# Kernel optimization log

Measured on AMD Instinct MI355X. Metric: run time of the kernel, lower is better.

The kernel has to match this reference:

```python
import jax, jax.numpy as jnp
import numpy as np

BETA = 0.5
THRESHOLD = 1e-12
NORM_EPS = 1e-12
SQRT_EPS = 1e-12


def _l2_normalize(x):
    # matches torch F.normalize(p=2, dim=1, eps=1e-12): x / max(||x||, eps)
    n = jnp.sqrt(jnp.sum(x * x, axis=1, keepdims=True))
    return x / jnp.maximum(n, NORM_EPS)


def _focal(d):
    # reg_method='log': log(beta*d + 1) if d > threshold else 0
    d_safe = jnp.where(d > THRESHOLD, d, THRESHOLD)
    return jnp.where(d > THRESHOLD, jnp.log(BETA * d_safe + 1.0), 0.0)


def setup_inputs() -> dict:
    key = jax.random.key(0)
    ks = jax.random.split(key, 6)
    B, D = 128, 512
    return {
        "x_audio": jax.random.normal(ks[0], (B, D), dtype=jnp.float32),
        "x_video": jax.random.normal(ks[1], (B, D), dtype=jnp.float32),
        "x_text": jax.random.normal(ks[2], (B, D), dtype=jnp.float32),
        "loss_audio": jax.random.uniform(ks[3], (), dtype=jnp.float32),
        "loss_video": jax.random.uniform(ks[4], (), dtype=jnp.float32),
        "loss_text": jax.random.uniform(ks[5], (), dtype=jnp.float32),
    }


def reference(x_audio, x_video, x_text, loss_audio, loss_video, loss_text):
    xs = [x_audio, x_video, x_text]
    losses = [loss_audio, loss_video, loss_text]
    R = len(xs)
    # L2-normalize each modality, then per-sample outer-product correlations [B, D, D]
    corr = [jnp.einsum('bi,bj->bij', xn, xn)
            for xn in (_l2_normalize(x) for x in xs)]
    ssa = []
    for m in range(R):
        acc = jnp.float32(0.0)
        for n in range(R):
            focal = _focal(losses[m] - losses[n])
            diff = corr[m] - corr[n]
            corr_diff = jnp.sqrt(SQRT_EPS + jnp.sum(diff * diff))
            acc = acc + focal * corr_diff
        ssa.append(acc)
    return jnp.stack(ssa)  # [R] ssa loss per modality
```

## Files before the change

### kernel.cpp

```cpp
#include <hip/hip_runtime.h>
#include <math.h>


#define SSA_BETA      0.5f
#define SSA_THRESHOLD 1e-12f
#define SSA_NORM_EPS  1e-12f
#define SSA_SQRT_EPS  1e-12f

static constexpr int SSA_B = 128;
static constexpr int SSA_D = 512;
static constexpr int SSA_NBLK = 32;
static constexpr int SSA_CTR_OFS = 512;

__global__ __launch_bounds__(256) void ssa_fused_kernel(
    const float* __restrict__ xa, const float* __restrict__ xv,
    const float* __restrict__ xt, const float* __restrict__ la,
    const float* __restrict__ lv, const float* __restrict__ lt,
    float* __restrict__ out, float* __restrict__ ws) {
  const int tid = threadIdx.x;
  const int wave = tid >> 6;
  const int lane = tid & 63;
  const int b = blockIdx.x * 4 + wave;

  const float4* pa = reinterpret_cast<const float4*>(xa + b * SSA_D);
  const float4* pv = reinterpret_cast<const float4*>(xv + b * SSA_D);
  const float4* pt = reinterpret_cast<const float4*>(xt + b * SSA_D);

  float sa = 0.f, sv = 0.f, st = 0.f;
  float dav = 0.f, dat = 0.f, dvt = 0.f;

#pragma unroll
  for (int k = 0; k < 2; ++k) {
    const int idx = lane + 64 * k;
    const float4 a = pa[idx];
    const float4 v = pv[idx];
    const float4 t = pt[idx];
    sa  += a.x * a.x + a.y * a.y + a.z * a.z + a.w * a.w;
    sv  += v.x * v.x + v.y * v.y + v.z * v.z + v.w * v.w;
    st  += t.x * t.x + t.y * t.y + t.z * t.z + t.w * t.w;
    dav += a.x * v.x + a.y * v.y + a.z * v.z + a.w * v.w;
    dat += a.x * t.x + a.y * t.y + a.z * t.z + a.w * t.w;
    dvt += v.x * t.x + v.y * t.y + v.z * t.z + v.w * t.w;
  }

#pragma unroll
  for (int off = 32; off > 0; off >>= 1) {
    sa  += __shfl_xor(sa, off);
    sv  += __shfl_xor(sv, off);
    st  += __shfl_xor(st, off);
    dav += __shfl_xor(dav, off);
    dat += __shfl_xor(dat, off);
    dvt += __shfl_xor(dvt, off);
  }

  __shared__ float sm[3][4];
  if (lane == 0) {
    const float na = fmaxf(sqrtf(sa), SSA_NORM_EPS);
    const float nv = fmaxf(sqrtf(sv), SSA_NORM_EPS);
    const float nt = fmaxf(sqrtf(st), SSA_NORM_EPS);
    const float na2 = sa / (na * na);
    const float nv2 = sv / (nv * nv);
    const float nt2 = st / (nt * nt);
    const float cav  = dav / (na * nv);
    const float cat_ = dat / (na * nt);
    const float cvt_ = dvt / (nv * nt);
    sm[0][wave] = na2 * na2 + nv2 * nv2 - 2.f * cav  * cav;
    sm[1][wave] = na2 * na2 + nt2 * nt2 - 2.f * cat_ * cat_;
    sm[2][wave] = nv2 * nv2 + nt2 * nt2 - 2.f * cvt_ * cvt_;
  }
  __syncthreads();

  if (wave != 0) return;

  unsigned int old = 0;
  if (lane == 0) {
    ws[0 * SSA_NBLK + blockIdx.x] = sm[0][0] + sm[0][1] + sm[0][2] + sm[0][3];
    ws[1 * SSA_NBLK + blockIdx.x] = sm[1][0] + sm[1][1] + sm[1][2] + sm[1][3];
    ws[2 * SSA_NBLK + blockIdx.x] = sm[2][0] + sm[2][1] + sm[2][2] + sm[2][3];
    __threadfence();
    old = atomicAdd(reinterpret_cast<unsigned int*>(ws + SSA_CTR_OFS), 1u);
  }
  old = __shfl(old, 0);
  if ((old & 31u) != 31u) return;

  __threadfence();

  float s0 = 0.f, s1 = 0.f, s2 = 0.f;
  if (lane < SSA_NBLK) {
    s0 = ws[0 * SSA_NBLK + lane];
    s1 = ws[1 * SSA_NBLK + lane];
    s2 = ws[2 * SSA_NBLK + lane];
  }
#pragma unroll
  for (int off = 16; off > 0; off >>= 1) {
    s0 += __shfl_xor(s0, off);
    s1 += __shfl_xor(s1, off);
    s2 += __shfl_xor(s2, off);
  }

  if (lane == 0) {
    const float dist01 = sqrtf(SSA_SQRT_EPS + s0);
    const float dist02 = sqrtf(SSA_SQRT_EPS + s1);
    const float dist12 = sqrtf(SSA_SQRT_EPS + s2);

    const float loss[3] = {la[0], lv[0], lt[0]};
    const float dist[3][3] = {{0.f, dist01, dist02},
                              {dist01, 0.f, dist12},
                              {dist02, dist12, 0.f}};
#pragma unroll
    for (int m = 0; m < 3; ++m) {
      float acc = 0.f;
#pragma unroll
      for (int n = 0; n < 3; ++n) {
        if (n == m) continue;
        const float d = loss[m] - loss[n];
        const float focal = (d > SSA_THRESHOLD) ? logf(SSA_BETA * d + 1.0f) : 0.f;
        acc += focal * dist[m][n];
      }
      out[m] = acc;
    }
  }
}

extern "C" void kernel_launch(void* const* d_in, const int* in_sizes, int n_in,
                              void* d_out, int out_size, void* d_ws, size_t ws_size,
                              hipStream_t stream) {
  const float* xa = (const float*)d_in[0];
  const float* xv = (const float*)d_in[1];
  const float* xt = (const float*)d_in[2];
  const float* la = (const float*)d_in[3];
  const float* lv = (const float*)d_in[4];
  const float* lt = (const float*)d_in[5];
  float* out = (float*)d_out;
  float* ws = (float*)d_ws;

  ssa_fused_kernel<<<SSA_NBLK, 256, 0, stream>>>(xa, xv, xt, la, lv, lt, out, ws);
}
```

Baseline: 9.753 us.

## Halve block count, hoist focal computation, and reset counter via memset

Launches 16 blocks of 512 threads (8 samples per block) instead of 32 blocks of 256, so fewer blocks take part in the last-block atomic reduction. The loss scalars and focal logs are computed early by every thread, overlapping with the vector loads instead of sitting on the serial tail of the last block. The per-block partial sums are reduced by shuffles, and the counter is now reset with a hipMemsetAsync before each launch. The exact-equality check on the counter replaces the modulo test. The extra memset node may add launch overhead that offsets the smaller tail work.

```diff
diff --git a/kernel.cpp b/kernel.cpp
--- a/kernel.cpp
+++ b/kernel.cpp
@@ -9,10 +9,10 @@
 
 static constexpr int SSA_B = 128;
 static constexpr int SSA_D = 512;
-static constexpr int SSA_NBLK = 32;
+static constexpr int SSA_NBLK = 16;
 static constexpr int SSA_CTR_OFS = 512;
 
-__global__ __launch_bounds__(256) void ssa_fused_kernel(
+__global__ __launch_bounds__(512) void ssa_fused_kernel(
     const float* __restrict__ xa, const float* __restrict__ xv,
     const float* __restrict__ xt, const float* __restrict__ la,
     const float* __restrict__ lv, const float* __restrict__ lt,
@@ -20,7 +20,9 @@
   const int tid = threadIdx.x;
   const int wave = tid >> 6;
   const int lane = tid & 63;
-  const int b = blockIdx.x * 4 + wave;
+  const int b = blockIdx.x * 8 + wave;
+
+  const float l0 = la[0], l1 = lv[0], l2 = lt[0];
 
   const float4* pa = reinterpret_cast<const float4*>(xa + b * SSA_D);
   const float4* pv = reinterpret_cast<const float4*>(xv + b * SSA_D);
@@ -43,6 +45,13 @@
     dvt += v.x * t.x + v.y * t.y + v.z * t.z + v.w * t.w;
   }
 
+  auto focal = [](float d) {
+    return (d > SSA_THRESHOLD) ? logf(SSA_BETA * d + 1.0f) : 0.f;
+  };
+  const float f01 = focal(l0 - l1), f10 = focal(l1 - l0);
+  const float f02 = focal(l0 - l2), f20 = focal(l2 - l0);
+  const float f12 = focal(l1 - l2), f21 = focal(l2 - l1);
+
 #pragma unroll
   for (int off = 32; off > 0; off >>= 1) {
     sa  += __shfl_xor(sa, off);
@@ -53,7 +62,7 @@
     dvt += __shfl_xor(dvt, off);
   }
 
-  __shared__ float sm[3][4];
+  __shared__ float sm[3][8];
   if (lane == 0) {
     const float na = fmaxf(sqrtf(sa), SSA_NORM_EPS);
     const float nv = fmaxf(sqrtf(sv), SSA_NORM_EPS);
@@ -72,16 +81,22 @@
 
   if (wave != 0) return;
 
+  const int pair = lane >> 3;
+  float pv_ = (pair < 3) ? sm[pair][lane & 7] : 0.f;
+#pragma unroll
+  for (int off = 4; off > 0; off >>= 1) pv_ += __shfl_xor(pv_, off);
+  if (pair < 3 && (lane & 7) == 0) {
+    ws[pair * SSA_NBLK + blockIdx.x] = pv_;
+  }
+
+  __threadfence();
+
   unsigned int old = 0;
   if (lane == 0) {
-    ws[0 * SSA_NBLK + blockIdx.x] = sm[0][0] + sm[0][1] + sm[0][2] + sm[0][3];
-    ws[1 * SSA_NBLK + blockIdx.x] = sm[1][0] + sm[1][1] + sm[1][2] + sm[1][3];
-    ws[2 * SSA_NBLK + blockIdx.x] = sm[2][0] + sm[2][1] + sm[2][2] + sm[2][3];
-    __threadfence();
     old = atomicAdd(reinterpret_cast<unsigned int*>(ws + SSA_CTR_OFS), 1u);
   }
   old = __shfl(old, 0);
-  if ((old & 31u) != 31u) return;
+  if (old != (unsigned int)(SSA_NBLK - 1)) return;
 
   __threadfence();
 
@@ -92,7 +107,7 @@
     s2 = ws[2 * SSA_NBLK + lane];
   }
 #pragma unroll
-  for (int off = 16; off > 0; off >>= 1) {
+  for (int off = 8; off > 0; off >>= 1) {
     s0 += __shfl_xor(s0, off);
     s1 += __shfl_xor(s1, off);
     s2 += __shfl_xor(s2, off);
@@ -102,23 +117,9 @@
     const float dist01 = sqrtf(SSA_SQRT_EPS + s0);
     const float dist02 = sqrtf(SSA_SQRT_EPS + s1);
     const float dist12 = sqrtf(SSA_SQRT_EPS + s2);
-
-    const float loss[3] = {la[0], lv[0], lt[0]};
-    const float dist[3][3] = {{0.f, dist01, dist02},
-                              {dist01, 0.f, dist12},
-                              {dist02, dist12, 0.f}};
-#pragma unroll
-    for (int m = 0; m < 3; ++m) {
-      float acc = 0.f;
-#pragma unroll
-      for (int n = 0; n < 3; ++n) {
-        if (n == m) continue;
-        const float d = loss[m] - loss[n];
-        const float focal = (d > SSA_THRESHOLD) ? logf(SSA_BETA * d + 1.0f) : 0.f;
-        acc += focal * dist[m][n];
-      }
-      out[m] = acc;
-    }
+    out[0] = f01 * dist01 + f02 * dist02;
+    out[1] = f10 * dist01 + f12 * dist12;
+    out[2] = f20 * dist02 + f21 * dist12;
   }
 }
 
@@ -134,5 +135,7 @@
   float* out = (float*)d_out;
   float* ws = (float*)d_ws;
 
-  ssa_fused_kernel<<<SSA_NBLK, 256, 0, stream>>>(xa, xv, xt, la, lv, lt, out, ws);
+  hipMemsetAsync((char*)d_ws + SSA_CTR_OFS * sizeof(float), 0,
+                 sizeof(unsigned int), stream);
+  ssa_fused_kernel<<<SSA_NBLK, 512, 0, stream>>>(xa, xv, xt, la, lv, lt, out, ws);
 }
```

Measured after the change: 14.67 us. 1.5x slower.
